# Kernel tuning notes

Hardware: AMD Instinct MI355X
Metric: run time of the kernel (lower is better)

The kernel has to match this reference:

```python
import jax, jax.numpy as jnp
import numpy as np

B, H, S, D = 4, 16, 2048, 64

def setup_inputs() -> dict:
    key = jax.random.key(0)
    kq, kk, kv = jax.random.split(key, 3)
    q = jax.random.normal(kq, (B, H, S, D), dtype=jnp.float32)
    k = jax.random.normal(kk, (B, H, S, D), dtype=jnp.float32)
    v = jax.random.normal(kv, (B, H, S, D), dtype=jnp.float32)
    # causal mask: True where attention is DISALLOWED (masked_fill semantics)
    row = jnp.arange(S)[:, None]
    col = jnp.arange(S)[None, :]
    attn_mask = (col > row)[None, None, :, :]  # [1,1,S,S] bool
    return {"q": q, "k": k, "v": v, "attn_mask": attn_mask}

def reference(q, k, v, attn_mask):
    scale = 1.0 / jnp.sqrt(jnp.float32(q.shape[-1]))
    # [B,H,S,S] scores
    scores = jnp.einsum("bhqd,bhkd->bhqk", q, k) * scale
    scores = jnp.where(attn_mask, -jnp.inf, scores)
    attn = jax.nn.softmax(scores, axis=-1)
    # dropout p=0 (eval) -> identity
    context = jnp.einsum("bhqk,bhkd->bhqd", attn, v)
    return context
```

## Files before the change

### kernel.cpp

```cpp
#include <hip/hip_runtime.h>

#define BB 4
#define HH 16
#define SS 2048
#define DD 64
#define KST 80

typedef __bf16 bf16x8 __attribute__((ext_vector_type(8)));
typedef __bf16 bf16x2 __attribute__((ext_vector_type(2)));
typedef float  f32x4  __attribute__((ext_vector_type(4)));
typedef unsigned short u16;
typedef unsigned int   u32;

__device__ __forceinline__ u16 f2bf(float f) {
    u32 u = __float_as_uint(f);
    u = (u + 0x7fffu + ((u >> 16) & 1u)) >> 16;
    return (u16)u;
}

__device__ __forceinline__ u32 pack2bf(float a, float b) {
#if __has_builtin(__builtin_amdgcn_cvt_pk_bf16_f32)
    bf16x2 t = __builtin_amdgcn_cvt_pk_bf16_f32(a, b);
    return __builtin_bit_cast(u32, t);
#else
    return (u32)f2bf(a) | ((u32)f2bf(b) << 16);
#endif
}

__global__ void prep(const float* __restrict__ q, const float* __restrict__ k,
                     const float* __restrict__ v,
                     u16* __restrict__ qbf, u16* __restrict__ kbf, u16* __restrict__ vt)
{
    __shared__ u16 tile[64 * 68];
    const int bh = blockIdx.y, s0 = blockIdx.x * 64, tid = threadIdx.x;
    const size_t base = (size_t)bh * SS * DD + (size_t)s0 * DD;
    const float qsc = 0.18033688011112042f;

    {
        const float4* qs4 = (const float4*)(q + base) + tid * 4;
        const float4* ks4 = (const float4*)(k + base) + tid * 4;
        union { u16 h[16]; uint4 u[2]; } oq, ok;
        #pragma unroll
        for (int j = 0; j < 4; ++j) {
            float4 a = qs4[j], b = ks4[j];
            oq.h[j*4+0] = f2bf(a.x * qsc); oq.h[j*4+1] = f2bf(a.y * qsc);
            oq.h[j*4+2] = f2bf(a.z * qsc); oq.h[j*4+3] = f2bf(a.w * qsc);
            ok.h[j*4+0] = f2bf(b.x); ok.h[j*4+1] = f2bf(b.y);
            ok.h[j*4+2] = f2bf(b.z); ok.h[j*4+3] = f2bf(b.w);
        }
        uint4* qd = (uint4*)(qbf + base) + tid * 2;
        uint4* kd = (uint4*)(kbf + base) + tid * 2;
        qd[0] = oq.u[0]; qd[1] = oq.u[1];
        kd[0] = ok.u[0]; kd[1] = ok.u[1];
    }
    {
        const int s4 = (tid >> 4) * 4;
        const int d4 = (tid & 15) * 4;
        float4 r0 = *(const float4*)(v + base + (size_t)(s4 + 0) * DD + d4);
        float4 r1 = *(const float4*)(v + base + (size_t)(s4 + 1) * DD + d4);
        float4 r2 = *(const float4*)(v + base + (size_t)(s4 + 2) * DD + d4);
        float4 r3 = *(const float4*)(v + base + (size_t)(s4 + 3) * DD + d4);
        const float c0[4] = {r0.x, r0.y, r0.z, r0.w};
        const float c1[4] = {r1.x, r1.y, r1.z, r1.w};
        const float c2[4] = {r2.x, r2.y, r2.z, r2.w};
        const float c3[4] = {r3.x, r3.y, r3.z, r3.w};
        #pragma unroll
        for (int i = 0; i < 4; ++i) {
            uint2 o;
            o.x = pack2bf(c0[i], c1[i]);
            o.y = pack2bf(c2[i], c3[i]);
            *(uint2*)(&tile[(d4 + i) * 68 + s4]) = o;
        }
    }
    __syncthreads();
    const int d  = tid >> 2;
    const int ch = tid & 3;
    uint4 o0 = *(const uint4*)(&tile[d * 68 + ch * 16]);
    uint4 o1 = *(const uint4*)(&tile[d * 68 + ch * 16 + 8]);
    u16* dst = vt + (size_t)bh * DD * SS + (size_t)d * SS + s0 + ch * 16;
    *(uint4*)(dst)     = o0;
    *(uint4*)(dst + 8) = o1;
}

__global__ __launch_bounds__(256, 3) void fa3(
    const u16* __restrict__ qbf, const u16* __restrict__ kbf,
    const u16* __restrict__ vtbf, float* __restrict__ out)
{
    const int tid  = threadIdx.x;
    const int lane = tid & 63;
    const int w    = tid >> 6;
    const int quad = lane >> 4;
    const int m16  = lane & 15;
    const int bx   = blockIdx.x;
    const int qblk = 15 - (bx >> 6);
    const int bh   = bx & 63;
    const size_t base  = (size_t)bh * SS * DD;
    const size_t vbase = (size_t)bh * DD * SS;
    const int qw0 = qblk * 128 + w * 32;

    __shared__ __align__(16) u16 Kt[2][64 * KST];
    __shared__ __align__(16) u16 Vt[2][64 * KST];
    __shared__ __align__(16) u16 Pt[4][16 * 64];

    bf16x8 qf[2][2];
    #pragma unroll
    for (int qs = 0; qs < 2; ++qs)
        #pragma unroll
        for (int dc = 0; dc < 2; ++dc)
            qf[qs][dc] = *(const bf16x8*)(qbf + base +
                (size_t)(qw0 + qs * 16 + m16) * DD + dc * 32 + quad * 8);

    const f32x4 vzero = {0.f, 0.f, 0.f, 0.f};
    f32x4 acc[2][4];
    float lrow[2] = {0.f, 0.f};
    #pragma unroll
    for (int qs = 0; qs < 2; ++qs)
        #pragma unroll
        for (int dt = 0; dt < 4; ++dt) acc[qs][dt] = vzero;

    const int ntiles = qblk * 2 + 2;
    const int sr = tid >> 3;
    const int sc = tid & 7;
    const u16* kp = kbf + base + (size_t)sr * DD + sc * 8;
    const u16* vp = vtbf + vbase + (size_t)sr * SS + sc * 8;

    {
        uint4 a0 = *(const uint4*)(kp);
        uint4 a1 = *(const uint4*)(kp + 32 * DD);
        uint4 b0 = *(const uint4*)(vp);
        uint4 b1 = *(const uint4*)(vp + 32 * SS);
        *(uint4*)(&Kt[0][sr * KST + sc * 8])        = a0;
        *(uint4*)(&Kt[0][(sr + 32) * KST + sc * 8]) = a1;
        *(uint4*)(&Vt[0][sr * KST + sc * 8])        = b0;
        *(uint4*)(&Vt[0][(sr + 32) * KST + sc * 8]) = b1;
    }

    for (int t = 0; t < ntiles; ++t) {
        const int kv0 = t * 64;
        const int cur = t & 1, nxt = cur ^ 1;
        __syncthreads();
        const bool haveNext = (t + 1 < ntiles);
        uint4 a0, a1, b0, b1;
        if (haveNext) {
            a0 = *(const uint4*)(kp + (size_t)(kv0 + 64) * DD);
            a1 = *(const uint4*)(kp + (size_t)(kv0 + 96) * DD);
            b0 = *(const uint4*)(vp + kv0 + 64);
            b1 = *(const uint4*)(vp + 32 * SS + kv0 + 64);
        }

        if (kv0 <= qw0 + 31) {
            bf16x8 kf[4][2], vf[4][2];
            #pragma unroll
            for (int st = 0; st < 4; ++st)
                #pragma unroll
                for (int dc = 0; dc < 2; ++dc) {
                    kf[st][dc] = *(const bf16x8*)(&Kt[cur][(st * 16 + m16) * KST + dc * 32 + quad * 8]);
                    vf[st][dc] = *(const bf16x8*)(&Vt[cur][(st * 16 + m16) * KST + dc * 32 + quad * 8]);
                }

            #pragma unroll
            for (int qs = 0; qs < 2; ++qs) {
                const int q0 = qw0 + qs * 16;
                if (kv0 > q0 + 15) continue;
                f32x4 s[4];
                #pragma unroll
                for (int st = 0; st < 4; ++st) {
                    s[st] = vzero;
                    #pragma unroll
                    for (int dc = 0; dc < 2; ++dc)
                        s[st] = __builtin_amdgcn_mfma_f32_16x16x32_bf16(
                            kf[st][dc], qf[qs][dc], s[st], 0, 0, 0);
                }
                if (kv0 + 63 > q0) {
                    const int qq = q0 + m16;
                    #pragma unroll
                    for (int st = 0; st < 4; ++st)
                        #pragma unroll
                        for (int r = 0; r < 4; ++r)
                            if (kv0 + st * 16 + quad * 4 + r > qq) s[st][r] = -1e30f;
                }
                float psum = 0.f;
                u32 pp[4][2];
                #pragma unroll
                for (int st = 0; st < 4; ++st) {
                    #pragma unroll
                    for (int r = 0; r < 4; ++r) {
                        const float p = __builtin_exp2f(s[st][r]);
                        s[st][r] = p;
                        psum += p;
                    }
                    pp[st][0] = pack2bf(s[st][0], s[st][1]);
                    pp[st][1] = pack2bf(s[st][2], s[st][3]);
                }
                lrow[qs] += psum;
                #pragma unroll
                for (int st = 0; st < 4; ++st) {
                    const int Gs = (st * 2 + (quad >> 1)) ^ (m16 & 7);
                    uint2 o; o.x = pp[st][0]; o.y = pp[st][1];
                    *(uint2*)(&Pt[w][m16 * 64 + Gs * 8 + (quad & 1) * 4]) = o;
                }
                #pragma unroll
                for (int kc = 0; kc < 2; ++kc) {
                    const int Gs = (kc * 4 + quad) ^ (m16 & 7);
                    const bf16x8 pf = *(const bf16x8*)(&Pt[w][m16 * 64 + Gs * 8]);
                    #pragma unroll
                    for (int dt = 0; dt < 4; ++dt)
                        acc[qs][dt] = __builtin_amdgcn_mfma_f32_16x16x32_bf16(
                            vf[dt][kc], pf, acc[qs][dt], 0, 0, 0);
                }
            }
        }

        if (haveNext) {
            *(uint4*)(&Kt[nxt][sr * KST + sc * 8])        = a0;
            *(uint4*)(&Kt[nxt][(sr + 32) * KST + sc * 8]) = a1;
            *(uint4*)(&Vt[nxt][sr * KST + sc * 8])        = b0;
            *(uint4*)(&Vt[nxt][(sr + 32) * KST + sc * 8]) = b1;
        }
    }

    #pragma unroll
    for (int qs = 0; qs < 2; ++qs) {
        float l = lrow[qs];
        l += __shfl_xor(l, 16);
        l += __shfl_xor(l, 32);
        const float inv = 1.f / l;
        const int qq = qw0 + qs * 16 + m16;
        #pragma unroll
        for (int dt = 0; dt < 4; ++dt) {
            float4 o = make_float4(acc[qs][dt][0] * inv, acc[qs][dt][1] * inv,
                                   acc[qs][dt][2] * inv, acc[qs][dt][3] * inv);
            *(float4*)(out + base + (size_t)qq * DD + dt * 16 + quad * 4) = o;
        }
    }
}

extern "C" void kernel_launch(void* const* d_in, const int* in_sizes, int n_in,
                              void* d_out, int out_size, void* d_ws, size_t ws_size,
                              hipStream_t stream)
{
    const float* q = (const float*)d_in[0];
    const float* k = (const float*)d_in[1];
    const float* v = (const float*)d_in[2];
    float* out = (float*)d_out;

    const size_t nelem = (size_t)BB * HH * SS * DD;
    u16* qbf  = (u16*)d_ws;
    u16* kbf  = qbf + nelem;
    u16* vtbf = kbf + nelem;

    prep<<<dim3(SS / 64, BB * HH), dim3(256), 0, stream>>>(q, k, v, qbf, kbf, vtbf);
    fa3<<<dim3(16 * 64), dim3(256), 0, stream>>>(qbf, kbf, vtbf, out);
}
```

Before: 236.1 us.

## Fuse bf16 conversion and V transpose into attention kernel, drop prep pass

Removes the separate prep kernel that converted Q/K/V to bf16 and transposed V into workspace. The attention kernel now loads fp32 Q, K and V directly, scales and packs Q into registers, and converts K and V into bf16 while staging them in shared memory, transposing V on the fly. This saves one kernel launch and the write and re-read of the bf16 workspace. In exchange, each tile reads twice as many bytes of K/V from global memory, repeated across query blocks, and adds conversion ALU work and more registers inside the main loop.

```diff
diff --git a/kernel.cpp b/kernel.cpp
--- a/kernel.cpp
+++ b/kernel.cpp
@@ -27,64 +27,16 @@
 #endif
 }
 
-__global__ void prep(const float* __restrict__ q, const float* __restrict__ k,
-                     const float* __restrict__ v,
-                     u16* __restrict__ qbf, u16* __restrict__ kbf, u16* __restrict__ vt)
-{
-    __shared__ u16 tile[64 * 68];
-    const int bh = blockIdx.y, s0 = blockIdx.x * 64, tid = threadIdx.x;
-    const size_t base = (size_t)bh * SS * DD + (size_t)s0 * DD;
-    const float qsc = 0.18033688011112042f;
-
-    {
-        const float4* qs4 = (const float4*)(q + base) + tid * 4;
-        const float4* ks4 = (const float4*)(k + base) + tid * 4;
-        union { u16 h[16]; uint4 u[2]; } oq, ok;
-        #pragma unroll
-        for (int j = 0; j < 4; ++j) {
-            float4 a = qs4[j], b = ks4[j];
-            oq.h[j*4+0] = f2bf(a.x * qsc); oq.h[j*4+1] = f2bf(a.y * qsc);
-            oq.h[j*4+2] = f2bf(a.z * qsc); oq.h[j*4+3] = f2bf(a.w * qsc);
-            ok.h[j*4+0] = f2bf(b.x); ok.h[j*4+1] = f2bf(b.y);
-            ok.h[j*4+2] = f2bf(b.z); ok.h[j*4+3] = f2bf(b.w);
-        }
-        uint4* qd = (uint4*)(qbf + base) + tid * 2;
-        uint4* kd = (uint4*)(kbf + base) + tid * 2;
-        qd[0] = oq.u[0]; qd[1] = oq.u[1];
-        kd[0] = ok.u[0]; kd[1] = ok.u[1];
-    }
-    {
-        const int s4 = (tid >> 4) * 4;
-        const int d4 = (tid & 15) * 4;
-        float4 r0 = *(const float4*)(v + base + (size_t)(s4 + 0) * DD + d4);
-        float4 r1 = *(const float4*)(v + base + (size_t)(s4 + 1) * DD + d4);
-        float4 r2 = *(const float4*)(v + base + (size_t)(s4 + 2) * DD + d4);
-        float4 r3 = *(const float4*)(v + base + (size_t)(s4 + 3) * DD + d4);
-        const float c0[4] = {r0.x, r0.y, r0.z, r0.w};
-        const float c1[4] = {r1.x, r1.y, r1.z, r1.w};
-        const float c2[4] = {r2.x, r2.y, r2.z, r2.w};
-        const float c3[4] = {r3.x, r3.y, r3.z, r3.w};
-        #pragma unroll
-        for (int i = 0; i < 4; ++i) {
-            uint2 o;
-            o.x = pack2bf(c0[i], c1[i]);
-            o.y = pack2bf(c2[i], c3[i]);
-            *(uint2*)(&tile[(d4 + i) * 68 + s4]) = o;
-        }
-    }
-    __syncthreads();
-    const int d  = tid >> 2;
-    const int ch = tid & 3;
-    uint4 o0 = *(const uint4*)(&tile[d * 68 + ch * 16]);
-    uint4 o1 = *(const uint4*)(&tile[d * 68 + ch * 16 + 8]);
-    u16* dst = vt + (size_t)bh * DD * SS + (size_t)d * SS + s0 + ch * 16;
-    *(uint4*)(dst)     = o0;
-    *(uint4*)(dst + 8) = o1;
-}
-
-__global__ __launch_bounds__(256, 3) void fa3(
-    const u16* __restrict__ qbf, const u16* __restrict__ kbf,
-    const u16* __restrict__ vtbf, float* __restrict__ out)
+__device__ __forceinline__ uint4 pack8(float4 a, float4 b) {
+    uint4 r;
+    r.x = pack2bf(a.x, a.y); r.y = pack2bf(a.z, a.w);
+    r.z = pack2bf(b.x, b.y); r.w = pack2bf(b.z, b.w);
+    return r;
+}
+
+__global__ __launch_bounds__(256, 3) void fa4(
+    const float* __restrict__ qg, const float* __restrict__ kg,
+    const float* __restrict__ vg, float* __restrict__ out)
 {
     const int tid  = threadIdx.x;
     const int lane = tid & 63;
@@ -94,9 +46,9 @@
     const int bx   = blockIdx.x;
     const int qblk = 15 - (bx >> 6);
     const int bh   = bx & 63;
-    const size_t base  = (size_t)bh * SS * DD;
-    const size_t vbase = (size_t)bh * DD * SS;
+    const size_t base = (size_t)bh * SS * DD;
     const int qw0 = qblk * 128 + w * 32;
+    const float qsc = 0.18033688011112042f;
 
     __shared__ __align__(16) u16 Kt[2][64 * KST];
     __shared__ __align__(16) u16 Vt[2][64 * KST];
@@ -106,9 +58,15 @@
     #pragma unroll
     for (int qs = 0; qs < 2; ++qs)
         #pragma unroll
-        for (int dc = 0; dc < 2; ++dc)
-            qf[qs][dc] = *(const bf16x8*)(qbf + base +
-                (size_t)(qw0 + qs * 16 + m16) * DD + dc * 32 + quad * 8);
+        for (int dc = 0; dc < 2; ++dc) {
+            const float* p = qg + base + (size_t)(qw0 + qs * 16 + m16) * DD + dc * 32 + quad * 8;
+            float4 a = *(const float4*)(p);
+            float4 b = *(const float4*)(p + 4);
+            a.x *= qsc; a.y *= qsc; a.z *= qsc; a.w *= qsc;
+            b.x *= qsc; b.y *= qsc; b.z *= qsc; b.w *= qsc;
+            uint4 u = pack8(a, b);
+            qf[qs][dc] = __builtin_bit_cast(bf16x8, u);
+        }
 
     const f32x4 vzero = {0.f, 0.f, 0.f, 0.f};
     f32x4 acc[2][4];
@@ -121,18 +79,29 @@
     const int ntiles = qblk * 2 + 2;
     const int sr = tid >> 3;
     const int sc = tid & 7;
-    const u16* kp = kbf + base + (size_t)sr * DD + sc * 8;
-    const u16* vp = vtbf + vbase + (size_t)sr * SS + sc * 8;
+    const float* kp = kg + base + (size_t)sr * DD + sc * 8;
+    const int vs4 = (tid & 15) * 4;
+    const int vd4 = (tid >> 4) * 4;
+    const float* vp = vg + base + (size_t)vs4 * DD + vd4;
 
     {
-        uint4 a0 = *(const uint4*)(kp);
-        uint4 a1 = *(const uint4*)(kp + 32 * DD);
-        uint4 b0 = *(const uint4*)(vp);
-        uint4 b1 = *(const uint4*)(vp + 32 * SS);
-        *(uint4*)(&Kt[0][sr * KST + sc * 8])        = a0;
-        *(uint4*)(&Kt[0][(sr + 32) * KST + sc * 8]) = a1;
-        *(uint4*)(&Vt[0][sr * KST + sc * 8])        = b0;
-        *(uint4*)(&Vt[0][(sr + 32) * KST + sc * 8]) = b1;
+        uint4 ka = pack8(*(const float4*)(kp),            *(const float4*)(kp + 4));
+        uint4 kb = pack8(*(const float4*)(kp + 32 * DD),  *(const float4*)(kp + 32 * DD + 4));
+        float4 r0 = *(const float4*)(vp);
+        float4 r1 = *(const float4*)(vp + DD);
+        float4 r2 = *(const float4*)(vp + 2 * DD);
+        float4 r3 = *(const float4*)(vp + 3 * DD);
+        *(uint4*)(&Kt[0][sr * KST + sc * 8])        = ka;
+        *(uint4*)(&Kt[0][(sr + 32) * KST + sc * 8]) = kb;
+        const float c0[4] = {r0.x, r0.y, r0.z, r0.w};
+        const float c1[4] = {r1.x, r1.y, r1.z, r1.w};
+        const float c2[4] = {r2.x, r2.y, r2.z, r2.w};
+        const float c3[4] = {r3.x, r3.y, r3.z, r3.w};
+        #pragma unroll
+        for (int i = 0; i < 4; ++i) {
+            uint2 o; o.x = pack2bf(c0[i], c1[i]); o.y = pack2bf(c2[i], c3[i]);
+            *(uint2*)(&Vt[0][(vd4 + i) * KST + vs4]) = o;
+        }
     }
 
     for (int t = 0; t < ntiles; ++t) {
@@ -140,12 +109,18 @@
         const int cur = t & 1, nxt = cur ^ 1;
         __syncthreads();
         const bool haveNext = (t + 1 < ntiles);
-        uint4 a0, a1, b0, b1;
+        float4 ka0, ka1, kb0, kb1, r0, r1, r2, r3;
         if (haveNext) {
-            a0 = *(const uint4*)(kp + (size_t)(kv0 + 64) * DD);
-            a1 = *(const uint4*)(kp + (size_t)(kv0 + 96) * DD);
-            b0 = *(const uint4*)(vp + kv0 + 64);
-            b1 = *(const uint4*)(vp + 32 * SS + kv0 + 64);
+            const float* kq = kp + (size_t)(kv0 + 64) * DD;
+            ka0 = *(const float4*)(kq);
+            ka1 = *(const float4*)(kq + 4);
+            kb0 = *(const float4*)(kq + 32 * DD);
+            kb1 = *(const float4*)(kq + 32 * DD + 4);
+            const float* vq = vp + (size_t)(kv0 + 64) * DD;
+            r0 = *(const float4*)(vq);
+            r1 = *(const float4*)(vq + DD);
+            r2 = *(const float4*)(vq + 2 * DD);
+            r3 = *(const float4*)(vq + 3 * DD);
         }
 
         if (kv0 <= qw0 + 31) {
@@ -212,10 +187,17 @@
         }
 
         if (haveNext) {
-            *(uint4*)(&Kt[nxt][sr * KST + sc * 8])        = a0;
-            *(uint4*)(&Kt[nxt][(sr + 32) * KST + sc * 8]) = a1;
-            *(uint4*)(&Vt[nxt][sr * KST + sc * 8])        = b0;
-            *(uint4*)(&Vt[nxt][(sr + 32) * KST + sc * 8]) = b1;
+            *(uint4*)(&Kt[nxt][sr * KST + sc * 8])        = pack8(ka0, ka1);
+            *(uint4*)(&Kt[nxt][(sr + 32) * KST + sc * 8]) = pack8(kb0, kb1);
+            const float c0[4] = {r0.x, r0.y, r0.z, r0.w};
+            const float c1[4] = {r1.x, r1.y, r1.z, r1.w};
+            const float c2[4] = {r2.x, r2.y, r2.z, r2.w};
+            const float c3[4] = {r3.x, r3.y, r3.z, r3.w};
+            #pragma unroll
+            for (int i = 0; i < 4; ++i) {
+                uint2 o; o.x = pack2bf(c0[i], c1[i]); o.y = pack2bf(c2[i], c3[i]);
+                *(uint2*)(&Vt[nxt][(vd4 + i) * KST + vs4]) = o;
+            }
         }
     }
 
@@ -244,11 +226,5 @@
     const float* v = (const float*)d_in[2];
     float* out = (float*)d_out;
 
-    const size_t nelem = (size_t)BB * HH * SS * DD;
-    u16* qbf  = (u16*)d_ws;
-    u16* kbf  = qbf + nelem;
-    u16* vtbf = kbf + nelem;
-
-    prep<<<dim3(SS / 64, BB * HH), dim3(256), 0, stream>>>(q, k, v, qbf, kbf, vtbf);
-    fa3<<<dim3(16 * 64), dim3(256), 0, stream>>>(qbf, kbf, vtbf, out);
-}
+    fa4<<<dim3(16 * 64), dim3(256), 0, stream>>>(q, k, v, out);
+}
```

Result: slower. 512.4 us (+117.0%).
